# Optimization experiments

Hardware: AMD Instinct MI355X
Metric: run time of the kernel (lower is better)

## Reference

```python
import jax, jax.numpy as jnp
import numpy as np

BN_EPS = 1e-5

def _conv1x1(x, w, b):
    # x: [B,C,H,W], w: [O,C], b: [O] -> [B,O,H,W]
    return jnp.einsum('bchw,oc->bohw', x, w) + b[None, :, None, None]

def setup_inputs() -> dict:
    key = jax.random.key(0)
    ks = jax.random.split(key, 9)
    B, C, H, W = 8, 256, 64, 64
    I = C // 2
    s_in = 1.0 / np.sqrt(C)
    s_out = 1.0 / np.sqrt(I)
    return {
        'x':       jax.random.normal(ks[0], (B, C, H, W), dtype=jnp.float32),
        'g_w':     jax.random.uniform(ks[1], (I, C), jnp.float32, -s_in, s_in),
        'g_b':     jax.random.uniform(ks[2], (I,),  jnp.float32, -s_in, s_in),
        'theta_w': jax.random.uniform(ks[3], (I, C), jnp.float32, -s_in, s_in),
        'theta_b': jax.random.uniform(ks[4], (I,),  jnp.float32, -s_in, s_in),
        'phi_w':   jax.random.uniform(ks[5], (I, C), jnp.float32, -s_in, s_in),
        'phi_b':   jax.random.uniform(ks[6], (I,),  jnp.float32, -s_in, s_in),
        'w_w':     jax.random.uniform(ks[7], (C, I), jnp.float32, -s_out, s_out),
        'w_b':     jax.random.uniform(ks[8], (C,),  jnp.float32, -s_out, s_out),
        'gamma':   jnp.ones((C,), dtype=jnp.float32),   # BN weight init constant 1
        'beta':    jnp.zeros((C,), dtype=jnp.float32),  # BN bias init constant 0
    }

def reference(x, g_w, g_b, theta_w, theta_b, phi_w, phi_b, w_w, w_b, gamma, beta):
    B, C, H, W = x.shape
    I = g_w.shape[0]
    N = H * W
    g_x     = _conv1x1(x, g_w, g_b).reshape(B, I, N)          # [B,I,N]
    theta_x = _conv1x1(x, theta_w, theta_b).reshape(B, I, N)  # [B,I,N]
    phi_x   = _conv1x1(x, phi_w, phi_b).reshape(B, I, N)      # [B,I,N]
    # f = theta^T @ phi : [B,N,N]
    f = jnp.einsum('bin,bim->bnm', theta_x, phi_x)
    a = jax.nn.softmax(f, axis=-1)
    # y = a @ g^T : [B,N,I] -> [B,I,H,W]
    y = jnp.einsum('bnm,bim->bin', a, g_x).reshape(B, I, H, W)
    wy = _conv1x1(y, w_w, w_b)                                # [B,C,H,W]
    # BatchNorm2d (training mode: batch statistics over B,H,W per channel)
    mean = jnp.mean(wy, axis=(0, 2, 3), keepdims=True)
    var = jnp.var(wy, axis=(0, 2, 3), keepdims=True)
    wy_bn = (wy - mean) * jax.lax.rsqrt(var + BN_EPS)
    wy_bn = wy_bn * gamma[None, :, None, None] + beta[None, :, None, None]
    return wy_bn + x
```

## Files before the change

kernel.cpp:

```cpp
#include <hip/hip_runtime.h>

#define B_ 8
#define C_ 256
#define I_ 128
#define N_ 4096
#define BN_ (B_ * N_)
#define LOG2E 1.4426950408889634f

typedef __attribute__((ext_vector_type(8))) short bf16x8;
typedef __attribute__((ext_vector_type(4))) float f32x4;
typedef __attribute__((ext_vector_type(4))) int i32x4;

static __device__ __forceinline__ short f2bf(float f) {
    unsigned u = __float_as_uint(f);
    unsigned r = u + 0x7fffu + ((u >> 16) & 1u);
    return (short)(r >> 16);
}
static __device__ __forceinline__ float bf2f(short s) {
    return __uint_as_float(((unsigned)(unsigned short)s) << 16);
}
static __device__ __forceinline__ unsigned cvt_pk_bf16(float lo, float hi) {
    unsigned r;
    asm("v_cvt_pk_bf16_f32 %0, %1, %2" : "=v"(r) : "v"(lo), "v"(hi));
    return r;
}

__global__ void k_prep(const float* g_w, const float* theta_w, const float* phi_w,
                       const float* g_b, const float* theta_b, const float* phi_b,
                       const float* w_w, short* wcat, short* wwb, float* bcat,
                       float* bnsum) {
    int i = blockIdx.x * 256 + threadIdx.x;
    if (i < 384 * 256) {
        int j = i >> 8, c = i & 255;
        float v = (j < 128) ? theta_w[j * 256 + c] * LOG2E
                : (j < 256) ? phi_w[(j - 128) * 256 + c]
                            : g_w[(j - 256) * 256 + c];
        wcat[i] = f2bf(v);
    } else if (i < 384 * 256 + 256 * 128) {
        int k = i - 384 * 256;
        wwb[k] = f2bf(w_w[k]);
    } else if (i < 384 * 256 + 256 * 128 + 384) {
        int j = i - (384 * 256 + 256 * 128);
        bcat[j] = (j < 128) ? theta_b[j] * LOG2E
                : (j < 256) ? phi_b[j - 128] : g_b[j - 256];
    } else if (i < 384 * 256 + 256 * 128 + 384 + 512) {
        bnsum[i - (384 * 256 + 256 * 128 + 384)] = 0.f;
    }
}

__global__ __launch_bounds__(256) void k_proj(const float* __restrict__ x,
                                              const short* __restrict__ wcat,
                                              const float* __restrict__ bcat,
                                              short* __restrict__ tp,
                                              short* __restrict__ gmat) {
    int b = blockIdx.y;
    int n0 = blockIdx.x * 64;
    int tid = threadIdx.x;
    int wave = tid >> 6, lane = tid & 63, s = lane & 15, q = lane >> 4;
    __shared__ __align__(16) char SM[33024];
    short (*xs)[258] = (short(*)[258])SM;

#pragma unroll
    for (int it = 0; it < 16; ++it) {
        int cr = (tid >> 4) + it * 16;
        int nc = tid & 15;
        const float4 v = *(const float4*)&x[((size_t)b * C_ + cr) * N_ + n0 + nc * 4];
        xs[nc * 4 + 0][cr] = f2bf(v.x);
        xs[nc * 4 + 1][cr] = f2bf(v.y);
        xs[nc * 4 + 2][cr] = f2bf(v.z);
        xs[nc * 4 + 3][cr] = f2bf(v.w);
    }
    __syncthreads();

    f32x4 acc[4][6];
#pragma unroll
    for (int rt = 0; rt < 4; ++rt)
#pragma unroll
        for (int jt = 0; jt < 6; ++jt) acc[rt][jt] = (f32x4){0.f, 0.f, 0.f, 0.f};

#pragma unroll
    for (int kb = 0; kb < 8; ++kb) {
        bf16x8 af[4], bfv[6];
#pragma unroll
        for (int rt = 0; rt < 4; ++rt)
            af[rt] = *(const bf16x8*)&xs[rt * 16 + s][kb * 32 + q * 8];
#pragma unroll
        for (int jt = 0; jt < 6; ++jt)
            bfv[jt] = *(const bf16x8*)&wcat[(wave * 96 + jt * 16 + s) * 256 + kb * 32 + q * 8];
#pragma unroll
        for (int rt = 0; rt < 4; ++rt)
#pragma unroll
            for (int jt = 0; jt < 6; ++jt)
                acc[rt][jt] = __builtin_amdgcn_mfma_f32_16x16x32_bf16(af[rt], bfv[jt], acc[rt][jt], 0, 0, 0);
    }
    __syncthreads();

    short* ytile = (short*)SM;
#pragma unroll
    for (int jt = 0; jt < 6; ++jt) {
        int j = wave * 96 + jt * 16 + s;
        if (j < 256) {
            float bias = bcat[j];
#pragma unroll
            for (int rt = 0; rt < 4; ++rt)
#pragma unroll
                for (int r = 0; r < 4; ++r)
                    ytile[(rt * 16 + 4 * q + r) * 256 + j] = f2bf(acc[rt][jt][r] + bias);
        }
    }
    __syncthreads();
    {
        short* dst = tp + ((size_t)b * N_ + n0) * 256;
#pragma unroll
        for (int k = 0; k < 8; ++k) {
            int off = k * 2048 + tid * 8;
            *(bf16x8*)(dst + off) = *(const bf16x8*)(ytile + off);
        }
    }
    __syncthreads();

    short* gt = (short*)SM;
#pragma unroll
    for (int jt = 0; jt < 6; ++jt) {
        int j = wave * 96 + jt * 16 + s;
        if (j >= 256) {
            float bias = bcat[j];
            int i2 = j - 256;
#pragma unroll
            for (int rt = 0; rt < 4; ++rt)
#pragma unroll
                for (int r = 0; r < 4; ++r)
                    gt[i2 * 66 + rt * 16 + 4 * q + r] = f2bf(acc[rt][jt][r] + bias);
        }
    }
    __syncthreads();
#pragma unroll
    for (int k = 0; k < 4; ++k) {
        int idx = k * 256 + tid;
        int i2 = idx >> 3, nch = idx & 7;
        bf16x8 v = *(const bf16x8*)(gt + i2 * 66 + nch * 8);
        *(bf16x8*)&gmat[((size_t)b * I_ + i2) * N_ + n0 + nch * 8] = v;
    }
}

__global__ __launch_bounds__(512, 2) void k_attn_wy(const short* __restrict__ tp,
                                                    const short* __restrict__ gmat,
                                                    const short* __restrict__ wwb,
                                                    const float* __restrict__ w_b,
                                                    short* __restrict__ wyh,
                                                    float* __restrict__ bnsum) {
    int id = blockIdx.x;
    int b = id & 7;
    int qt = id >> 3;
    int n0 = qt * 128;
    int tid = threadIdx.x;
    int wave = tid >> 6, lane = tid & 63, s = lane & 15, q = lane >> 4;
    int kg = wave >> 2, qg = wave & 3;

    __shared__ __align__(16) short SH[65536];
    __shared__ float l_lds[2][128];
    char* base = (char*)SH;

    const int swz = (s & 7) << 4;
    int kA[4];
#pragma unroll
    for (int kb = 0; kb < 4; ++kb) kA[kb] = s * 256 + ((kb * 64 + q * 16) ^ swz);
    int vA[2];
#pragma unroll
    for (int kb2 = 0; kb2 < 2; ++kb2) vA[kb2] = s * 256 + ((kb2 * 64 + q * 16) ^ swz);
    int krow = tid >> 4, kch = tid & 15;
    int stW = krow * 256 + ((kch * 16) ^ ((krow & 7) << 4));

    i32x4 onesw = (i32x4){0x3F803F80, 0x3F803F80, 0x3F803F80, 0x3F803F80};
    bf16x8 vone = __builtin_bit_cast(bf16x8, onesw);

    bf16x8 qf[2][4];
#pragma unroll
    for (int fr = 0; fr < 2; ++fr) {
        const short* qb = tp + ((size_t)b * N_ + n0 + qg * 32 + fr * 16 + s) * 256;
#pragma unroll
        for (int kb = 0; kb < 4; ++kb) qf[fr][kb] = *(const bf16x8*)(qb + kb * 32 + q * 8);
    }

    f32x4 ot[2][8];
#pragma unroll
    for (int fr = 0; fr < 2; ++fr)
#pragma unroll
        for (int t = 0; t < 8; ++t) ot[fr][t] = (f32x4){0.f, 0.f, 0.f, 0.f};
    f32x4 lacc[2] = {(f32x4){0.f, 0.f, 0.f, 0.f}, (f32x4){0.f, 0.f, 0.f, 0.f}};

    bf16x8 pk[4], pv[4];
#pragma unroll
    for (int it = 0; it < 4; ++it) {
        pk[it] = *(const bf16x8*)&tp[((size_t)b * N_ + krow + it * 32) * 256 + 128 + kch * 8];
        pv[it] = *(const bf16x8*)&gmat[((size_t)b * I_ + krow + it * 32) * N_ + kch * 8];
    }
#pragma unroll
    for (int it = 0; it < 4; ++it) {
        *(bf16x8*)(base + stW + it * 8192) = pk[it];
        *(bf16x8*)(base + 32768 + stW + it * 8192) = pv[it];
    }
    __syncthreads();

    const int hK = kg * 16384, hV = kg * 128;

    for (int i = 0; i < 32; ++i) {
        char* KtB = base + (i & 1) * 65536;
        char* VtB = KtB + 32768;
        if (i < 31) {
            size_t m = (size_t)(i + 1) * 128;
#pragma unroll
            for (int it = 0; it < 4; ++it) {
                pk[it] = *(const bf16x8*)&tp[((size_t)b * N_ + m + krow + it * 32) * 256 + 128 + kch * 8];
                pv[it] = *(const bf16x8*)&gmat[((size_t)b * I_ + krow + it * 32) * N_ + m + kch * 8];
            }
        }

        f32x4 sa[2][4];
#pragma unroll
        for (int fr = 0; fr < 2; ++fr)
#pragma unroll
            for (int tc = 0; tc < 4; ++tc) sa[fr][tc] = (f32x4){0.f, 0.f, 0.f, 0.f};
        __builtin_amdgcn_s_setprio(1);
#pragma unroll
        for (int tc = 0; tc < 4; ++tc) {
            bf16x8 bfv[4];
#pragma unroll
            for (int kb = 0; kb < 4; ++kb)
                bfv[kb] = *(const bf16x8*)(KtB + hK + kA[kb] + tc * 4096);
#pragma unroll
            for (int fr = 0; fr < 2; ++fr)
#pragma unroll
                for (int kb = 0; kb < 4; ++kb)
                    sa[fr][tc] = __builtin_amdgcn_mfma_f32_16x16x32_bf16(bfv[kb], qf[fr][kb], sa[fr][tc], 0, 0, 0);
        }
        __builtin_amdgcn_s_setprio(0);

        unsigned W[2][4][2];
#pragma unroll
        for (int fr = 0; fr < 2; ++fr) {
#pragma unroll
            for (int tc = 0; tc < 4; ++tc)
#pragma unroll
                for (int r = 0; r < 4; ++r) sa[fr][tc][r] = exp2f(sa[fr][tc][r]);
#pragma unroll
            for (int tc = 0; tc < 4; ++tc) {
                W[fr][tc][0] = cvt_pk_bf16(sa[fr][tc][0], sa[fr][tc][1]);
                W[fr][tc][1] = cvt_pk_bf16(sa[fr][tc][2], sa[fr][tc][3]);
            }
        }

#pragma unroll
        for (int kb2 = 0; kb2 < 2; ++kb2) {
            bf16x8 pa[2];
#pragma unroll
            for (int fr = 0; fr < 2; ++fr) {
                unsigned rA = W[fr][2 * kb2 + 0][0];
                unsigned rB = W[fr][2 * kb2 + 0][1];
                unsigned rC = W[fr][2 * kb2 + 1][0];
                unsigned rD = W[fr][2 * kb2 + 1][1];
                asm("v_permlane32_swap_b32 %0, %1" : "+v"(rA), "+v"(rC));
                asm("v_permlane32_swap_b32 %0, %1" : "+v"(rB), "+v"(rD));
                asm("v_permlane16_swap_b32 %0, %1" : "+v"(rA), "+v"(rC));
                asm("v_permlane16_swap_b32 %0, %1" : "+v"(rB), "+v"(rD));
                i32x4 wv = (i32x4){(int)rA, (int)rB, (int)rC, (int)rD};
                pa[fr] = __builtin_bit_cast(bf16x8, wv);
            }
            __builtin_amdgcn_s_setprio(1);
            lacc[0] = __builtin_amdgcn_mfma_f32_16x16x32_bf16(pa[0], vone, lacc[0], 0, 0, 0);
            lacc[1] = __builtin_amdgcn_mfma_f32_16x16x32_bf16(pa[1], vone, lacc[1], 0, 0, 0);
#pragma unroll
            for (int t = 0; t < 8; ++t) {
                bf16x8 vb = *(const bf16x8*)(VtB + hV + vA[kb2] + t * 4096);
                ot[0][t] = __builtin_amdgcn_mfma_f32_16x16x32_bf16(pa[0], vb, ot[0][t], 0, 0, 0);
                ot[1][t] = __builtin_amdgcn_mfma_f32_16x16x32_bf16(pa[1], vb, ot[1][t], 0, 0, 0);
            }
            __builtin_amdgcn_s_setprio(0);
        }

        if (i < 31) {
            char* KtN = base + ((i & 1) ^ 1) * 65536;
#pragma unroll
            for (int it = 0; it < 4; ++it) {
                *(bf16x8*)(KtN + stW + it * 8192) = pk[it];
                *(bf16x8*)(KtN + 32768 + stW + it * 8192) = pv[it];
            }
        }
        __syncthreads();
    }

    if (s == 0) {
#pragma unroll
        for (int fr = 0; fr < 2; ++fr)
#pragma unroll
            for (int r = 0; r < 4; ++r)
                l_lds[kg][qg * 32 + fr * 16 + 4 * q + r] = lacc[fr][r];
    }
    if (kg == 1) {
#pragma unroll
        for (int fr = 0; fr < 2; ++fr)
#pragma unroll
            for (int t = 0; t < 8; ++t)
#pragma unroll
                for (int r = 0; r < 4; ++r) {
                    int row = qg * 32 + fr * 16 + 4 * q + r;
                    int colb = (t * 16 + s) * 4;
                    *(float*)(base + row * 512 + (colb ^ ((row & 7) << 4))) = ot[fr][t][r];
                }
    }
    __syncthreads();
    if (kg == 0) {
#pragma unroll
        for (int fr = 0; fr < 2; ++fr)
#pragma unroll
            for (int t = 0; t < 8; ++t)
#pragma unroll
                for (int r = 0; r < 4; ++r) {
                    int row = qg * 32 + fr * 16 + 4 * q + r;
                    int colb = (t * 16 + s) * 4;
                    float p = *(const float*)(base + row * 512 + (colb ^ ((row & 7) << 4)));
                    float v = ot[fr][t][r] + p;
                    int byt = 65536 + row * 256 + (((t * 16 + s) * 2) ^ ((row & 7) << 4));
                    *(short*)(base + byt) = f2bf(v);
                }
    }
    __syncthreads();

    f32x4 acc[2][8];
#pragma unroll
    for (int ct = 0; ct < 2; ++ct)
#pragma unroll
        for (int jt = 0; jt < 8; ++jt) acc[ct][jt] = (f32x4){0.f, 0.f, 0.f, 0.f};
#pragma unroll
    for (int kb = 0; kb < 4; ++kb) {
        bf16x8 af[2];
#pragma unroll
        for (int ct = 0; ct < 2; ++ct)
            af[ct] = *(const bf16x8*)&wwb[(wave * 32 + ct * 16 + s) * 128 + kb * 32 + q * 8];
#pragma unroll
        for (int jt = 0; jt < 8; ++jt) {
            bf16x8 yb = *(const bf16x8*)(base + 65536 + kA[kb] + jt * 4096);
#pragma unroll
            for (int ct = 0; ct < 2; ++ct)
                acc[ct][jt] = __builtin_amdgcn_mfma_f32_16x16x32_bf16(af[ct], yb, acc[ct][jt], 0, 0, 0);
        }
    }
    float linv[8];
#pragma unroll
    for (int jt = 0; jt < 8; ++jt)
        linv[jt] = 1.0f / (l_lds[0][jt * 16 + s] + l_lds[1][jt * 16 + s]);
#pragma unroll
    for (int ct = 0; ct < 2; ++ct)
#pragma unroll
        for (int r = 0; r < 4; ++r) {
            int c = wave * 32 + ct * 16 + 4 * q + r;
            float bias = w_b[c];
            float s1 = 0.f, s2 = 0.f;
#pragma unroll
            for (int jt = 0; jt < 8; ++jt) {
                float v = acc[ct][jt][r] * linv[jt] + bias;
                short w = f2bf(v);
                wyh[((size_t)b * C_ + c) * N_ + n0 + jt * 16 + s] = w;
                float vr = bf2f(w);
                s1 += vr;
                s2 += vr * vr;
            }
#pragma unroll
            for (int off = 1; off < 16; off <<= 1) {
                s1 += __shfl_xor(s1, off);
                s2 += __shfl_xor(s2, off);
            }
            if (s == 0) {
                atomicAdd(&bnsum[c], s1);
                atomicAdd(&bnsum[256 + c], s2);
            }
        }
}

__global__ __launch_bounds__(256) void k_out(const short* __restrict__ wyh,
                                             const float* __restrict__ x,
                                             const float* __restrict__ bnsum,
                                             const float* __restrict__ gamma,
                                             const float* __restrict__ beta,
                                             float* __restrict__ out) {
    int gid = blockIdx.x * 256 + threadIdx.x;
    size_t base = (size_t)gid * 8;
    int c = (int)((base >> 12) & 255);
    const float inv = 1.0f / 32768.0f;
    float mean = bnsum[c] * inv;
    float var = bnsum[256 + c] * inv - mean * mean;
    float sc = gamma[c] * rsqrtf(var + 1e-5f);
    float sh = beta[c] - mean * sc;
    bf16x8 w = *(const bf16x8*)&wyh[base];
    float4 x0 = *(const float4*)&x[base];
    float4 x1 = *(const float4*)&x[base + 4];
    float4 o0, o1;
    o0.x = bf2f(w[0]) * sc + sh + x0.x;
    o0.y = bf2f(w[1]) * sc + sh + x0.y;
    o0.z = bf2f(w[2]) * sc + sh + x0.z;
    o0.w = bf2f(w[3]) * sc + sh + x0.w;
    o1.x = bf2f(w[4]) * sc + sh + x1.x;
    o1.y = bf2f(w[5]) * sc + sh + x1.y;
    o1.z = bf2f(w[6]) * sc + sh + x1.z;
    o1.w = bf2f(w[7]) * sc + sh + x1.w;
    *(float4*)&out[base] = o0;
    *(float4*)&out[base + 4] = o1;
}

extern "C" void kernel_launch(void* const* d_in, const int* in_sizes, int n_in,
                              void* d_out, int out_size, void* d_ws, size_t ws_size,
                              hipStream_t stream) {
    const float* x       = (const float*)d_in[0];
    const float* g_w     = (const float*)d_in[1];
    const float* g_b     = (const float*)d_in[2];
    const float* theta_w = (const float*)d_in[3];
    const float* theta_b = (const float*)d_in[4];
    const float* phi_w   = (const float*)d_in[5];
    const float* phi_b   = (const float*)d_in[6];
    const float* w_w     = (const float*)d_in[7];
    const float* w_b     = (const float*)d_in[8];
    const float* gamma   = (const float*)d_in[9];
    const float* beta    = (const float*)d_in[10];

    char* ws = (char*)d_ws;
    size_t off = 0;
    auto alloc = [&](size_t bytes) {
        void* p = ws + off;
        off += (bytes + 255) & ~(size_t)255;
        return p;
    };
    short*  wcat  = (short*)alloc((size_t)384 * 256 * 2);
    short*  wwb   = (short*)alloc((size_t)256 * 128 * 2);
    float*  bcat  = (float*)alloc((size_t)384 * 4);
    float*  bnsum = (float*)alloc(512 * 4);
    short*  tp    = (short*)alloc((size_t)BN_ * 256 * 2);
    short*  gmat  = (short*)alloc((size_t)B_ * I_ * N_ * 2);
    short*  wyh   = (short*)alloc((size_t)BN_ * C_ * 2);

    k_prep<<<516, 256, 0, stream>>>(g_w, theta_w, phi_w, g_b, theta_b, phi_b, w_w,
                                    wcat, wwb, bcat, bnsum);
    k_proj<<<dim3(64, 8), 256, 0, stream>>>(x, wcat, bcat, tp, gmat);
    k_attn_wy<<<256, 512, 0, stream>>>(tp, gmat, wwb, w_b, wyh, bnsum);
    k_out<<<4096, 256, 0, stream>>>(wyh, x, bnsum, gamma, beta, (float*)d_out);
}
```

Measured before the change: 244.9 us.

## Load K/V fragments directly from global memory and replace BN atomics with partials

The attention loop no longer stages K and V tiles through double-buffered LDS with a block barrier every step. Each wave now loads its MFMA fragments straight from global memory (via L2), and each key-group wave set walks its own half of the keys. BatchNorm sums are written as per-block partials and reduced by a new small k_fin kernel instead of global atomicAdd, and the zeroing in k_prep is removed. This trades LDS traffic and syncs for uncoalesced, redundant global loads across waves, and adds one kernel launch.

```diff
diff --git a/kernel.cpp b/kernel.cpp
--- a/kernel.cpp
+++ b/kernel.cpp
@@ -27,8 +27,7 @@
 
 __global__ void k_prep(const float* g_w, const float* theta_w, const float* phi_w,
                        const float* g_b, const float* theta_b, const float* phi_b,
-                       const float* w_w, short* wcat, short* wwb, float* bcat,
-                       float* bnsum) {
+                       const float* w_w, short* wcat, short* wwb, float* bcat) {
     int i = blockIdx.x * 256 + threadIdx.x;
     if (i < 384 * 256) {
         int j = i >> 8, c = i & 255;
@@ -43,8 +42,6 @@
         int j = i - (384 * 256 + 256 * 128);
         bcat[j] = (j < 128) ? theta_b[j] * LOG2E
                 : (j < 256) ? phi_b[j - 128] : g_b[j - 256];
-    } else if (i < 384 * 256 + 256 * 128 + 384 + 512) {
-        bnsum[i - (384 * 256 + 256 * 128 + 384)] = 0.f;
     }
 }
 
@@ -148,7 +145,7 @@
                                                     const short* __restrict__ wwb,
                                                     const float* __restrict__ w_b,
                                                     short* __restrict__ wyh,
-                                                    float* __restrict__ bnsum) {
+                                                    float* __restrict__ bnpart) {
     int id = blockIdx.x;
     int b = id & 7;
     int qt = id >> 3;
@@ -157,19 +154,13 @@
     int wave = tid >> 6, lane = tid & 63, s = lane & 15, q = lane >> 4;
     int kg = wave >> 2, qg = wave & 3;
 
-    __shared__ __align__(16) short SH[65536];
+    __shared__ __align__(16) short SH[49152];
     __shared__ float l_lds[2][128];
     char* base = (char*)SH;
-
     const int swz = (s & 7) << 4;
     int kA[4];
 #pragma unroll
     for (int kb = 0; kb < 4; ++kb) kA[kb] = s * 256 + ((kb * 64 + q * 16) ^ swz);
-    int vA[2];
-#pragma unroll
-    for (int kb2 = 0; kb2 < 2; ++kb2) vA[kb2] = s * 256 + ((kb2 * 64 + q * 16) ^ swz);
-    int krow = tid >> 4, kch = tid & 15;
-    int stW = krow * 256 + ((kch * 16) ^ ((krow & 7) << 4));
 
     i32x4 onesw = (i32x4){0x3F803F80, 0x3F803F80, 0x3F803F80, 0x3F803F80};
     bf16x8 vone = __builtin_bit_cast(bf16x8, onesw);
@@ -182,6 +173,9 @@
         for (int kb = 0; kb < 4; ++kb) qf[fr][kb] = *(const bf16x8*)(qb + kb * 32 + q * 8);
     }
 
+    const short* kTp = tp + ((size_t)b * N_ + kg * 2048 + s) * 256 + 128 + q * 8;
+    const short* vGp = gmat + ((size_t)b * I_ + s) * N_ + kg * 2048 + q * 8;
+
     f32x4 ot[2][8];
 #pragma unroll
     for (int fr = 0; fr < 2; ++fr)
@@ -189,32 +183,8 @@
         for (int t = 0; t < 8; ++t) ot[fr][t] = (f32x4){0.f, 0.f, 0.f, 0.f};
     f32x4 lacc[2] = {(f32x4){0.f, 0.f, 0.f, 0.f}, (f32x4){0.f, 0.f, 0.f, 0.f}};
 
-    bf16x8 pk[4], pv[4];
-#pragma unroll
-    for (int it = 0; it < 4; ++it) {
-        pk[it] = *(const bf16x8*)&tp[((size_t)b * N_ + krow + it * 32) * 256 + 128 + kch * 8];
-        pv[it] = *(const bf16x8*)&gmat[((size_t)b * I_ + krow + it * 32) * N_ + kch * 8];
-    }
-#pragma unroll
-    for (int it = 0; it < 4; ++it) {
-        *(bf16x8*)(base + stW + it * 8192) = pk[it];
-        *(bf16x8*)(base + 32768 + stW + it * 8192) = pv[it];
-    }
-    __syncthreads();
-
-    const int hK = kg * 16384, hV = kg * 128;
-
-    for (int i = 0; i < 32; ++i) {
-        char* KtB = base + (i & 1) * 65536;
-        char* VtB = KtB + 32768;
-        if (i < 31) {
-            size_t m = (size_t)(i + 1) * 128;
-#pragma unroll
-            for (int it = 0; it < 4; ++it) {
-                pk[it] = *(const bf16x8*)&tp[((size_t)b * N_ + m + krow + it * 32) * 256 + 128 + kch * 8];
-                pv[it] = *(const bf16x8*)&gmat[((size_t)b * I_ + krow + it * 32) * N_ + m + kch * 8];
-            }
-        }
+    for (int step = 0; step < 32; ++step) {
+        int mloc = step * 64;
 
         f32x4 sa[2][4];
 #pragma unroll
@@ -224,15 +194,15 @@
         __builtin_amdgcn_s_setprio(1);
 #pragma unroll
         for (int tc = 0; tc < 4; ++tc) {
-            bf16x8 bfv[4];
-#pragma unroll
-            for (int kb = 0; kb < 4; ++kb)
-                bfv[kb] = *(const bf16x8*)(KtB + hK + kA[kb] + tc * 4096);
+            const short* kp = kTp + (size_t)(mloc + tc * 16) * 256;
+            bf16x8 kf[4];
+#pragma unroll
+            for (int kb = 0; kb < 4; ++kb) kf[kb] = *(const bf16x8*)(kp + kb * 32);
 #pragma unroll
             for (int fr = 0; fr < 2; ++fr)
 #pragma unroll
                 for (int kb = 0; kb < 4; ++kb)
-                    sa[fr][tc] = __builtin_amdgcn_mfma_f32_16x16x32_bf16(bfv[kb], qf[fr][kb], sa[fr][tc], 0, 0, 0);
+                    sa[fr][tc] = __builtin_amdgcn_mfma_f32_16x16x32_bf16(kf[kb], qf[fr][kb], sa[fr][tc], 0, 0, 0);
         }
         __builtin_amdgcn_s_setprio(0);
 
@@ -250,9 +220,9 @@
             }
         }
 
-#pragma unroll
-        for (int kb2 = 0; kb2 < 2; ++kb2) {
-            bf16x8 pa[2];
+        bf16x8 pa[2][2];
+#pragma unroll
+        for (int kb2 = 0; kb2 < 2; ++kb2)
 #pragma unroll
             for (int fr = 0; fr < 2; ++fr) {
                 unsigned rA = W[fr][2 * kb2 + 0][0];
@@ -264,29 +234,26 @@
                 asm("v_permlane16_swap_b32 %0, %1" : "+v"(rA), "+v"(rC));
                 asm("v_permlane16_swap_b32 %0, %1" : "+v"(rB), "+v"(rD));
                 i32x4 wv = (i32x4){(int)rA, (int)rB, (int)rC, (int)rD};
-                pa[fr] = __builtin_bit_cast(bf16x8, wv);
+                pa[fr][kb2] = __builtin_bit_cast(bf16x8, wv);
             }
-            __builtin_amdgcn_s_setprio(1);
-            lacc[0] = __builtin_amdgcn_mfma_f32_16x16x32_bf16(pa[0], vone, lacc[0], 0, 0, 0);
-            lacc[1] = __builtin_amdgcn_mfma_f32_16x16x32_bf16(pa[1], vone, lacc[1], 0, 0, 0);
-#pragma unroll
-            for (int t = 0; t < 8; ++t) {
-                bf16x8 vb = *(const bf16x8*)(VtB + hV + vA[kb2] + t * 4096);
-                ot[0][t] = __builtin_amdgcn_mfma_f32_16x16x32_bf16(pa[0], vb, ot[0][t], 0, 0, 0);
-                ot[1][t] = __builtin_amdgcn_mfma_f32_16x16x32_bf16(pa[1], vb, ot[1][t], 0, 0, 0);
-            }
-            __builtin_amdgcn_s_setprio(0);
-        }
-
-        if (i < 31) {
-            char* KtN = base + ((i & 1) ^ 1) * 65536;
-#pragma unroll
-            for (int it = 0; it < 4; ++it) {
-                *(bf16x8*)(KtN + stW + it * 8192) = pk[it];
-                *(bf16x8*)(KtN + 32768 + stW + it * 8192) = pv[it];
-            }
-        }
-        __syncthreads();
+
+        __builtin_amdgcn_s_setprio(1);
+        lacc[0] = __builtin_amdgcn_mfma_f32_16x16x32_bf16(pa[0][0], vone, lacc[0], 0, 0, 0);
+        lacc[1] = __builtin_amdgcn_mfma_f32_16x16x32_bf16(pa[1][0], vone, lacc[1], 0, 0, 0);
+        lacc[0] = __builtin_amdgcn_mfma_f32_16x16x32_bf16(pa[0][1], vone, lacc[0], 0, 0, 0);
+        lacc[1] = __builtin_amdgcn_mfma_f32_16x16x32_bf16(pa[1][1], vone, lacc[1], 0, 0, 0);
+
+#pragma unroll
+        for (int t = 0; t < 8; ++t) {
+            const short* vp = vGp + (size_t)(t * 16) * N_ + mloc;
+            bf16x8 vb0 = *(const bf16x8*)(vp);
+            bf16x8 vb1 = *(const bf16x8*)(vp + 32);
+            ot[0][t] = __builtin_amdgcn_mfma_f32_16x16x32_bf16(pa[0][0], vb0, ot[0][t], 0, 0, 0);
+            ot[1][t] = __builtin_amdgcn_mfma_f32_16x16x32_bf16(pa[1][0], vb0, ot[1][t], 0, 0, 0);
+            ot[0][t] = __builtin_amdgcn_mfma_f32_16x16x32_bf16(pa[0][1], vb1, ot[0][t], 0, 0, 0);
+            ot[1][t] = __builtin_amdgcn_mfma_f32_16x16x32_bf16(pa[1][1], vb1, ot[1][t], 0, 0, 0);
+        }
+        __builtin_amdgcn_s_setprio(0);
     }
 
     if (s == 0) {
@@ -371,10 +338,23 @@
                 s2 += __shfl_xor(s2, off);
             }
             if (s == 0) {
-                atomicAdd(&bnsum[c], s1);
-                atomicAdd(&bnsum[256 + c], s2);
+                bnpart[(size_t)c * 256 + id] = s1;
+                bnpart[(size_t)(256 + c) * 256 + id] = s2;
             }
         }
+}
+
+__global__ __launch_bounds__(256) void k_fin(const float* __restrict__ bnpart,
+                                             float* __restrict__ bnsum) {
+    int j = blockIdx.x * 256 + threadIdx.x;
+    const float4* p = (const float4*)(bnpart + (size_t)j * 256);
+    float s = 0.f;
+#pragma unroll
+    for (int k = 0; k < 64; ++k) {
+        float4 v = p[k];
+        s += (v.x + v.y) + (v.z + v.w);
+    }
+    bnsum[j] = s;
 }
 
 __global__ __launch_bounds__(256) void k_out(const short* __restrict__ wyh,
@@ -429,17 +409,19 @@
         off += (bytes + 255) & ~(size_t)255;
         return p;
     };
-    short*  wcat  = (short*)alloc((size_t)384 * 256 * 2);
-    short*  wwb   = (short*)alloc((size_t)256 * 128 * 2);
-    float*  bcat  = (float*)alloc((size_t)384 * 4);
-    float*  bnsum = (float*)alloc(512 * 4);
-    short*  tp    = (short*)alloc((size_t)BN_ * 256 * 2);
-    short*  gmat  = (short*)alloc((size_t)B_ * I_ * N_ * 2);
-    short*  wyh   = (short*)alloc((size_t)BN_ * C_ * 2);
-
-    k_prep<<<516, 256, 0, stream>>>(g_w, theta_w, phi_w, g_b, theta_b, phi_b, w_w,
-                                    wcat, wwb, bcat, bnsum);
+    short*  wcat   = (short*)alloc((size_t)384 * 256 * 2);
+    short*  wwb    = (short*)alloc((size_t)256 * 128 * 2);
+    float*  bcat   = (float*)alloc((size_t)384 * 4);
+    float*  bnsum  = (float*)alloc(512 * 4);
+    float*  bnpart = (float*)alloc((size_t)512 * 256 * 4);
+    short*  tp     = (short*)alloc((size_t)BN_ * 256 * 2);
+    short*  gmat   = (short*)alloc((size_t)B_ * I_ * N_ * 2);
+    short*  wyh    = (short*)alloc((size_t)BN_ * C_ * 2);
+
+    k_prep<<<514, 256, 0, stream>>>(g_w, theta_w, phi_w, g_b, theta_b, phi_b, w_w,
+                                    wcat, wwb, bcat);
     k_proj<<<dim3(64, 8), 256, 0, stream>>>(x, wcat, bcat, tp, gmat);
-    k_attn_wy<<<256, 512, 0, stream>>>(tp, gmat, wwb, w_b, wyh, bnsum);
+    k_attn_wy<<<256, 512, 0, stream>>>(tp, gmat, wwb, w_b, wyh, bnpart);
+    k_fin<<<2, 256, 0, stream>>>(bnpart, bnsum);
     k_out<<<4096, 256, 0, stream>>>(wyh, x, bnsum, gamma, beta, (float*)d_out);
 }
```

Result: slower. 381.3 us (+55.7%).
